# Kernel tuning notes

Hardware: AMD Instinct MI355X
Metric: run time of the kernel (lower is better)

## Reference

```python
import jax, jax.numpy as jnp
import numpy as np

N = 8
IN_F = 64
OUT_F = 64
BATCH = 16
SEQ = 8192


def setup_inputs() -> dict:
    key = jax.random.key(0)
    k_x, k_a, k_s = jax.random.split(key, 3)
    x = jax.random.normal(k_x, (BATCH, SEQ, IN_F, N), dtype=jnp.float32)
    A = jax.random.normal(k_a, (N, N, N), dtype=jnp.float32) * 0.1
    # xavier_normal_ on view(n*out_features, in_features): std = sqrt(2/(fan_in+fan_out))
    std = float(np.sqrt(2.0 / (IN_F + N * OUT_F)))
    S = jax.random.normal(k_s, (N, OUT_F, IN_F), dtype=jnp.float32) * std
    bias = jnp.zeros((OUT_F * N,), dtype=jnp.float32)
    return {"x": x, "A": A, "S": S, "bias": bias}


def reference(x, A, S, bias):
    n = N
    out_f, in_f = S.shape[1], S.shape[2]
    batch_shape = x.shape[:-2]
    # H[a,b,c,d] = sum_i A[i,a,c] * S[i,b,d]; reshape rows=(a,b), cols=(c,d)
    H = jnp.einsum('iac,ibd->abcd', A, S).reshape(n * out_f, n * in_f)
    x_flat = x.reshape(*batch_shape, in_f * n)
    out_flat = x_flat @ H.T + bias  # [..., n*out_f]
    return out_flat.reshape(*batch_shape, out_f, n)
```

## Files before the change

kernel.cpp:

```cpp
#include <hip/hip_runtime.h>
#include <hip/hip_bf16.h>


#define MDIM (16 * 8192)
#define KD 512
#define ND 512
#define BM 128
#define BN 128
#define BK 32

typedef __attribute__((ext_vector_type(8))) short short8;
typedef __attribute__((ext_vector_type(4))) float f32x4;

__device__ __forceinline__ unsigned pack2_bf16(float x, float y) {
    union { __hip_bfloat162 h; unsigned u; } cv;
    cv.h = __float22bfloat162_rn(make_float2(x, y));
    return cv.u;
}

__device__ __forceinline__ short8 cvt_frag(f32x4 a, f32x4 b) {
    union { unsigned u[4]; short8 s; } r;
    r.u[0] = pack2_bf16(a.x, a.y);
    r.u[1] = pack2_bf16(a.z, a.w);
    r.u[2] = pack2_bf16(b.x, b.y);
    r.u[3] = pack2_bf16(b.z, b.w);
    return r.s;
}

__device__ __forceinline__ void async16(const void* g, void* l) {
    __builtin_amdgcn_global_load_lds(
        (const __attribute__((address_space(1))) unsigned*)g,
        (__attribute__((address_space(3))) unsigned*)l, 16, 0, 0);
}

__global__ void build_h(const float* __restrict__ A, const float* __restrict__ S,
                        __hip_bfloat16* __restrict__ H) {
    int idx = blockIdx.x * 256 + threadIdx.x;
    int j = idx >> 9, k = idx & 511;
    int a = j >> 6, b = j & 63, c = k >> 6, d = k & 63;
    float acc = 0.f;
#pragma unroll
    for (int i = 0; i < 8; ++i)
        acc += A[i * 64 + a * 8 + c] * S[i * 4096 + b * 64 + d];
    H[idx] = __float2bfloat16(acc);
}

__global__ __launch_bounds__(256)
void phm_gemm(const float* __restrict__ X, const __hip_bfloat16* __restrict__ Hm,
              const float* __restrict__ bias, float* __restrict__ out) {
    __shared__ float As[BM * BK];
    __shared__ __hip_bfloat16 Bs[BN * BK];

    const int tid = threadIdx.x;
    const int m0 = blockIdx.y * BM;
    const int n0 = blockIdx.x * BN;

    const float* ag[4]; void* al[4];
#pragma unroll
    for (int q = 0; q < 4; ++q) {
        int seg = q * 256 + tid;
        int row = seg >> 3;
        int c16 = (seg & 7) ^ (row & 7);
        ag[q] = X + (size_t)(m0 + row) * KD + c16 * 4;
        al[q] = (char*)As + seg * 16;
    }
    const __hip_bfloat16* bg[2]; void* bl[2];
#pragma unroll
    for (int q = 0; q < 2; ++q) {
        int seg = q * 256 + tid;
        int row = seg >> 2;
        int c16 = seg & 3;
        bg[q] = Hm + (size_t)(n0 + row) * KD + c16 * 8;
        bl[q] = (char*)Bs + seg * 16;
    }

    const int wave = tid >> 6, lane = tid & 63;
    const int wm = (wave >> 1) * 64, wn = (wave & 1) * 64;
    const int fr = lane & 15;
    const int fs = lane >> 4;
    const int ca = (2 * fs) ^ (fr & 7);
    const int cb = ca ^ 1;

    f32x4 acc[4][4];
#pragma unroll
    for (int i = 0; i < 4; ++i)
#pragma unroll
        for (int j = 0; j < 4; ++j) acc[i][j] = (f32x4)(0.f);

    for (int kt = 0; kt < KD / BK; ++kt) {
#pragma unroll
        for (int q = 0; q < 4; ++q) async16(ag[q] + kt * BK, al[q]);
#pragma unroll
        for (int q = 0; q < 2; ++q) async16(bg[q] + kt * BK, bl[q]);
        __syncthreads();

        short8 bfr[4];
#pragma unroll
        for (int ni = 0; ni < 4; ++ni)
            bfr[ni] = *(const short8*)(Bs + (wn + ni * 16 + fr) * BK + fs * 8);

#pragma unroll
        for (int mi = 0; mi < 4; ++mi) {
            const float* rp = As + (wm + mi * 16 + fr) * BK;
            f32x4 a0 = *(const f32x4*)(rp + ca * 4);
            f32x4 a1 = *(const f32x4*)(rp + cb * 4);
            short8 afr = cvt_frag(a0, a1);
#pragma unroll
            for (int ni = 0; ni < 4; ++ni)
                acc[mi][ni] = __builtin_amdgcn_mfma_f32_16x16x32_bf16(
                    afr, bfr[ni], acc[mi][ni], 0, 0, 0);
        }
        __syncthreads();
    }

    const int cm = wm + fs * 4;
    const int cn0 = n0 + wn + fr;
#pragma unroll
    for (int mi = 0; mi < 4; ++mi) {
#pragma unroll
        for (int ni = 0; ni < 4; ++ni) {
            int col = cn0 + ni * 16;
            float bv = bias[col];
            float* op = out + (size_t)(m0 + cm + mi * 16) * ND + col;
#pragma unroll
            for (int r = 0; r < 4; ++r)
                op[(size_t)r * ND] = acc[mi][ni][r] + bv;
        }
    }
}

extern "C" void kernel_launch(void* const* d_in, const int* in_sizes, int n_in,
                              void* d_out, int out_size, void* d_ws, size_t ws_size,
                              hipStream_t stream) {
    const float* x    = (const float*)d_in[0];
    const float* A    = (const float*)d_in[1];
    const float* S    = (const float*)d_in[2];
    const float* bias = (const float*)d_in[3];
    float* out = (float*)d_out;
    __hip_bfloat16* H = (__hip_bfloat16*)d_ws;

    build_h<<<dim3(512 * 512 / 256), dim3(256), 0, stream>>>(A, S, H);
    phm_gemm<<<dim3(ND / BN, MDIM / BM), dim3(256), 0, stream>>>(x, H, bias, out);
}
```

Before: 519.6 us.

## Double-buffer LDS tiles, remap blocks per XCD, swizzle B tile layout

Splits shared memory into two buffers so the async global-to-LDS loads for the next K tile are issued while MFMAs consume the current one, and drops the trailing barrier. Switches to a 1D grid whose block index is remapped so consecutive work items sharing X rows land on the same XCD, improving L2 reuse. Adds an XOR swizzle to the B tile LDS layout to cut bank conflicts on fragment reads. Doubles LDS use per block, which may reduce occupancy.

```diff
diff --git a/kernel.cpp b/kernel.cpp
--- a/kernel.cpp
+++ b/kernel.cpp
@@ -8,6 +8,10 @@
 #define BM 128
 #define BN 128
 #define BK 32
+#define NKT (KD / BK)
+#define ABYTES (BM * BK * 4)
+#define BBYTES (BN * BK * 2)
+#define BUFBYTES (ABYTES + BBYTES)
 
 typedef __attribute__((ext_vector_type(8))) short short8;
 typedef __attribute__((ext_vector_type(4))) float f32x4;
@@ -48,30 +52,33 @@
 __global__ __launch_bounds__(256)
 void phm_gemm(const float* __restrict__ X, const __hip_bfloat16* __restrict__ Hm,
               const float* __restrict__ bias, float* __restrict__ out) {
-    __shared__ float As[BM * BK];
-    __shared__ __hip_bfloat16 Bs[BN * BK];
+    __shared__ __align__(16) char smem[2][BUFBYTES];
 
     const int tid = threadIdx.x;
-    const int m0 = blockIdx.y * BM;
-    const int n0 = blockIdx.x * BN;
 
-    const float* ag[4]; void* al[4];
+    const int b = blockIdx.x;
+    const int xcd = b & 7, slot = b >> 3;
+    const int work = xcd * 512 + slot;
+    const int m0 = (work >> 2) * BM;
+    const int n0 = (work & 3) * BN;
+
+    const float* ag[4]; int asl[4];
 #pragma unroll
     for (int q = 0; q < 4; ++q) {
         int seg = q * 256 + tid;
         int row = seg >> 3;
         int c16 = (seg & 7) ^ (row & 7);
         ag[q] = X + (size_t)(m0 + row) * KD + c16 * 4;
-        al[q] = (char*)As + seg * 16;
+        asl[q] = seg * 16;
     }
-    const __hip_bfloat16* bg[2]; void* bl[2];
+    const __hip_bfloat16* bg[2]; int bsl[2];
 #pragma unroll
     for (int q = 0; q < 2; ++q) {
         int seg = q * 256 + tid;
         int row = seg >> 2;
-        int c16 = seg & 3;
+        int c16 = (seg & 3) ^ ((row >> 1) & 3);
         bg[q] = Hm + (size_t)(n0 + row) * KD + c16 * 8;
-        bl[q] = (char*)Bs + seg * 16;
+        bsl[q] = ABYTES + seg * 16;
     }
 
     const int wave = tid >> 6, lane = tid & 63;
@@ -79,7 +86,7 @@
     const int fr = lane & 15;
     const int fs = lane >> 4;
     const int ca = (2 * fs) ^ (fr & 7);
-    const int cb = ca ^ 1;
+    const int bslot = fs ^ ((fr >> 1) & 3);
 
     f32x4 acc[4][4];
 #pragma unroll
@@ -87,30 +94,41 @@
 #pragma unroll
         for (int j = 0; j < 4; ++j) acc[i][j] = (f32x4)(0.f);
 
-    for (int kt = 0; kt < KD / BK; ++kt) {
 #pragma unroll
-        for (int q = 0; q < 4; ++q) async16(ag[q] + kt * BK, al[q]);
+    for (int q = 0; q < 4; ++q) async16(ag[q], smem[0] + asl[q]);
 #pragma unroll
-        for (int q = 0; q < 2; ++q) async16(bg[q] + kt * BK, bl[q]);
+    for (int q = 0; q < 2; ++q) async16(bg[q], smem[0] + bsl[q]);
+
+    for (int kt = 0; kt < NKT; ++kt) {
         __syncthreads();
 
+        if (kt + 1 < NKT) {
+            char* dst = smem[(kt + 1) & 1];
+#pragma unroll
+            for (int q = 0; q < 4; ++q) async16(ag[q] + (kt + 1) * BK, dst + asl[q]);
+#pragma unroll
+            for (int q = 0; q < 2; ++q) async16(bg[q] + (kt + 1) * BK, dst + bsl[q]);
+        }
+
+        const char* buf = smem[kt & 1];
         short8 bfr[4];
 #pragma unroll
-        for (int ni = 0; ni < 4; ++ni)
-            bfr[ni] = *(const short8*)(Bs + (wn + ni * 16 + fr) * BK + fs * 8);
+        for (int ni = 0; ni < 4; ++ni) {
+            int row = wn + ni * 16 + fr;
+            bfr[ni] = *(const short8*)(buf + ABYTES + row * 64 + bslot * 16);
+        }
 
 #pragma unroll
         for (int mi = 0; mi < 4; ++mi) {
-            const float* rp = As + (wm + mi * 16 + fr) * BK;
+            const float* rp = (const float*)(buf) + (wm + mi * 16 + fr) * BK;
             f32x4 a0 = *(const f32x4*)(rp + ca * 4);
-            f32x4 a1 = *(const f32x4*)(rp + cb * 4);
+            f32x4 a1 = *(const f32x4*)(rp + (ca ^ 1) * 4);
             short8 afr = cvt_frag(a0, a1);
 #pragma unroll
             for (int ni = 0; ni < 4; ++ni)
                 acc[mi][ni] = __builtin_amdgcn_mfma_f32_16x16x32_bf16(
                     afr, bfr[ni], acc[mi][ni], 0, 0, 0);
         }
-        __syncthreads();
     }
 
     const int cm = wm + fs * 4;
@@ -140,5 +158,5 @@
     __hip_bfloat16* H = (__hip_bfloat16*)d_ws;
 
     build_h<<<dim3(512 * 512 / 256), dim3(256), 0, stream>>>(A, S, H);
-    phm_gemm<<<dim3(ND / BN, MDIM / BM), dim3(256), 0, stream>>>(x, H, bias, out);
+    phm_gemm<<<dim3(MDIM / BM * (ND / BN)), dim3(256), 0, stream>>>(x, H, bias, out);
 }
```

Result: no change. 526.9 us (+1.4%).
